# Kernel optimization log

Measured on AMD Instinct MI355X. Metric: run time of the kernel, lower is better.

The kernel has to match this reference:

```python
import jax, jax.numpy as jnp
import numpy as np
from jax import lax

B, C, H, W = 32, 64, 112, 112
ALPHA, BETA1, BETA2 = 0.25, 1.0, 1.0

# STE sign for weights (DifferntiableSign): fwd = +/-1, bwd mask |w|<=1 (w in [-1,1))
@jax.custom_vjp
def dsign(w):
    return jnp.where(w >= 0, 1.0, -1.0).astype(w.dtype)
def _dsign_fwd(w):
    return dsign(w), w
def _dsign_bwd(w, g):
    return (g * ((w < 1) & (w >= -1)).astype(g.dtype),)
dsign.defvjp(_dsign_fwd, _dsign_bwd)

# ReActNet BinaryActivation: fwd = sign(x), bwd piecewise-polynomial STE
@jax.custom_vjp
def bin_act(x):
    return jnp.where(x >= 0, 1.0, -1.0).astype(x.dtype)
def _ba_fwd(x):
    return bin_act(x), x
def _ba_bwd(x, g):
    slope = jnp.where((x >= -1) & (x < 0), 2.0 + 2.0 * x,
             jnp.where((x >= 0) & (x < 1), 2.0 - 2.0 * x, 0.0))
    return (g * slope.astype(g.dtype),)
bin_act.defvjp(_ba_fwd, _ba_bwd)

def scaled_sign_conv(x, w):
    # per-output-channel scale = mean(|w|) over (in, kh, kw)
    scale = jnp.mean(jnp.abs(w), axis=(1, 2, 3), keepdims=True)
    wb = scale * dsign(w)
    return lax.conv_general_dilated(x, wb, window_strides=(1, 1),
                                    padding=((1, 1), (1, 1)),
                                    dimension_numbers=("NCHW", "OIHW", "NCHW"))

def add_bias(x, b):
    return x + b[None, :, None, None]

def prelu(x, a):
    return jnp.where(x >= 0, x, a[None, :, None, None] * x)

def setup_inputs() -> dict:
    key = jax.random.key(0)
    ks = jax.random.split(key, 12)
    x = jax.random.normal(ks[0], (B, C, H, W), dtype=jnp.float32)
    # conv weights: symmetric uniform in [-1e-3, 1e-3] so signs are nontrivial
    w3 = (jax.random.uniform(ks[1], (C, C, 3, 3)) - 0.5) * 0.002
    w_pw = (jax.random.uniform(ks[2], (C, C, 3, 3)) - 0.5) * 0.002
    b11 = jax.random.normal(ks[3], (C,)) * 0.01
    b12 = jax.random.normal(ks[4], (C,)) * 0.01
    b13 = jax.random.normal(ks[5], (C,)) * 0.01
    b21 = jax.random.normal(ks[6], (C,)) * 0.01
    b22 = jax.random.normal(ks[7], (C,)) * 0.01
    b23 = jax.random.normal(ks[8], (C,)) * 0.01
    a1 = jax.random.uniform(ks[9], (C,), minval=0.1, maxval=0.4)
    a2 = jax.random.uniform(ks[10], (C,), minval=0.1, maxval=0.4)
    return {"x": x, "w3": w3, "w_pw": w_pw, "b11": b11, "b12": b12, "b13": b13,
            "b21": b21, "b22": b22, "b23": b23, "a1": a1, "a2": a2}

def reference(x, w3, w_pw, b11, b12, b13, b21, b22, b23, a1, a2):
    x_in = x * BETA1
    out1 = add_bias(x_in, b11)            # move11
    out1 = bin_act(out1)
    out1 = scaled_sign_conv(out1, w3)     # binary_3x3
    out1 = x + out1 * ALPHA               # stride==1: residual is original x
    out1 = add_bias(out1, b12)            # move12
    out1 = prelu(out1, a1)
    out1 = add_bias(out1, b13)            # move13
    out1_in = out1 * BETA2
    out2 = add_bias(out1_in, b21)         # move21
    out2 = bin_act(out2)
    out2 = scaled_sign_conv(out2, w_pw)   # binary_pw (3x3 per given defaults)
    out2 = out2 * ALPHA + out1
    out2 = add_bias(out2, b22)            # move22
    out2 = prelu(out2, a2)
    out2 = add_bias(out2, b23)            # move23
    return out2
```

## Files before the change

### kernel.cpp

```cpp
#include <hip/hip_runtime.h>
#include <hip/hip_fp16.h>
#include <stdint.h>

#define Bn 32
#define Cc 64
#define Hh 112
#define Ww 112
#define HWp (Hh*Ww)
#define NPIX (Bn*HWp)
#define PW 114
#define PHW (PW*PW)
#define ALPHA 0.25f

#define WB1_OFF   0
#define WB2_OFF   4608
#define ASC1_OFF  9216
#define ASC2_OFF  9472
#define CI1_OFF   9728
#define CI2_OFF   12032
#define BITS1_OFF 16384
#define BITS2_OFF (16384 + 3326976)
#define OUT1H_OFF (16384 + 2*3326976)
#define WS_NEED   (OUT1H_OFF + (size_t)NPIX*Cc*2)

__global__ __launch_bounds__(64) void prep_weights(
        const float* __restrict__ w3, const float* __restrict__ wpw,
        uint64_t* __restrict__ wb1, uint64_t* __restrict__ wb2,
        float* __restrict__ asc1, float* __restrict__ asc2,
        int* __restrict__ ci1, int* __restrict__ ci2) {
    int b = blockIdx.x;
    int lane = threadIdx.x;
    const float* w  = (b < 64) ? w3   : wpw;
    uint64_t* wbits = (b < 64) ? wb1  : wb2;
    float*    ascp  = (b < 64) ? asc1 : asc2;
    int*      cip   = (b < 64) ? ci1  : ci2;
    int o = b & 63;
    const float* wp = w + ((size_t)o * Cc + lane) * 9;
    float v[9]; float asum = 0.f;
    #pragma unroll
    for (int t = 0; t < 9; ++t) { v[t] = wp[t]; asum += fabsf(v[t]); }
    uint64_t bal[9];
    #pragma unroll
    for (int t = 0; t < 9; ++t) bal[t] = __ballot(v[t] < 0.f);
    if (lane < 9) {
        wbits[o * 9 + lane] = bal[lane];
        int ty = lane, tr = ty / 3, tc = ty % 3;
        int sum = 0;
        #pragma unroll
        for (int t = 0; t < 9; ++t) {
            int r = t / 3, c = t % 3;
            bool inv = (tr == 0 && r == 0) || (tr == 2 && r == 2) ||
                       (tc == 0 && c == 0) || (tc == 2 && c == 2);
            if (inv) sum += 64 - 2 * (int)__popcll(bal[t]);
        }
        cip[o * 9 + ty] = 576 - sum;
    }
    #pragma unroll
    for (int off = 32; off > 0; off >>= 1) asum += __shfl_down(asum, off, 64);
    if (lane == 0) ascp[o] = ALPHA * asum * (1.f / 576.f);
}

__global__ __launch_bounds__(256) void pack1(const float* __restrict__ x,
                                             const float* __restrict__ b11,
                                             uint64_t* __restrict__ bits1,
                                             uint64_t* __restrict__ bits2) {
    int pc = blockIdx.x * 256 + threadIdx.x;
    if (pc >= PHW) return;
    int n = blockIdx.y;
    int ph = pc / PW, pw = pc - ph * PW;
    size_t bi = (size_t)n * PHW + pc;
    if (ph == 0 || ph == PW - 1 || pw == 0 || pw == PW - 1) {
        bits1[bi] = 0; bits2[bi] = 0;
        return;
    }
    int hw = (ph - 1) * Ww + (pw - 1);
    const float* xp = x + (size_t)n * Cc * HWp + hw;
    uint64_t m = 0;
    #pragma unroll 1
    for (int cc = 0; cc < Cc; cc += 16) {
        float v[16];
        #pragma unroll
        for (int j = 0; j < 16; ++j) v[j] = xp[(size_t)(cc + j) * HWp];
        #pragma unroll
        for (int j = 0; j < 16; ++j)
            if (v[j] + b11[cc + j] < 0.f) m |= (1ull << (cc + j));
    }
    bits1[bi] = m;
}

template <typename OutT>
__global__ __launch_bounds__(256) void conv1_ep(
        const float* __restrict__ x, const uint64_t* __restrict__ bits1,
        const uint64_t* __restrict__ wb, const float* __restrict__ asc,
        const int* __restrict__ cint,
        const float* __restrict__ b12, const float* __restrict__ a1,
        const float* __restrict__ b13, const float* __restrict__ b21,
        OutT* __restrict__ out1, uint64_t* __restrict__ bits2) {
    __shared__ int lci[Cc * 12];
    for (int i = threadIdx.x; i < Cc * 9; i += 256) {
        int o = i / 9, ty = i - o * 9;
        lci[o * 12 + ty] = cint[i];
    }
    __syncthreads();

    int hw = blockIdx.x * 256 + threadIdx.x;
    int n = blockIdx.y;
    int h = hw / Ww, w = hw - h * Ww;
    int t9 = ((h == 0) ? 0 : (h == Hh - 1) ? 6 : 3) +
             ((w == 0) ? 0 : (w == Ww - 1) ? 2 : 1);

    const uint64_t* bp = bits1 + (size_t)n * PHW + (h + 1) * PW + (w + 1);
    uint64_t w00 = bp[-PW - 1], w01 = bp[-PW], w02 = bp[-PW + 1];
    uint64_t w10 = bp[-1],      w11 = bp[0],   w12 = bp[1];
    uint64_t w20 = bp[PW - 1],  w21 = bp[PW],  w22 = bp[PW + 1];

    const float* xp = x + (size_t)n * Cc * HWp + hw;
    OutT* op = out1 + (size_t)n * Cc * HWp + hw;
    uint64_t m2 = 0;

    float xv[8], xn[8];
    #pragma unroll
    for (int j = 0; j < 8; ++j) xv[j] = xp[(size_t)j * HWp];

    #pragma unroll 1
    for (int oc = 0; oc < Cc; oc += 8) {
        #pragma unroll
        for (int j = 0; j < 8; ++j) xn[j] = xp[(size_t)((oc + 8 + j) & 63) * HWp];
        #pragma unroll
        for (int j = 0; j < 8; ++j) {
            int o = oc + j;
            const uint64_t* wo = wb + o * 9;
            int s;
            s  = (int)__popcll(w00 ^ wo[0]);
            s += (int)__popcll(w01 ^ wo[1]);
            s += (int)__popcll(w02 ^ wo[2]);
            s += (int)__popcll(w10 ^ wo[3]);
            s += (int)__popcll(w11 ^ wo[4]);
            s += (int)__popcll(w12 ^ wo[5]);
            s += (int)__popcll(w20 ^ wo[6]);
            s += (int)__popcll(w21 ^ wo[7]);
            s += (int)__popcll(w22 ^ wo[8]);
            int m = lci[o * 12 + t9] - (s << 1);
            float v = fmaf(asc[o], (float)m, xv[j]);
            v += b12[o];
            v = v >= 0.f ? v : a1[o] * v;
            v += b13[o];
            op[(size_t)o * HWp] = (OutT)v;
            if (v + b21[o] < 0.f) m2 |= (1ull << o);
        }
        #pragma unroll
        for (int j = 0; j < 8; ++j) xv[j] = xn[j];
    }
    bits2[(size_t)n * PHW + (h + 1) * PW + (w + 1)] = m2;
}

template <typename InT>
__global__ __launch_bounds__(256) void conv2_ep(
        const uint64_t* __restrict__ bits2, const InT* __restrict__ out1,
        const uint64_t* __restrict__ wb, const float* __restrict__ asc,
        const int* __restrict__ cint,
        const float* __restrict__ b22, const float* __restrict__ a2,
        const float* __restrict__ b23, float* __restrict__ out) {
    __shared__ int lci[Cc * 12];
    for (int i = threadIdx.x; i < Cc * 9; i += 256) {
        int o = i / 9, ty = i - o * 9;
        lci[o * 12 + ty] = cint[i];
    }
    __syncthreads();

    int hw = blockIdx.x * 256 + threadIdx.x;
    int n = blockIdx.y;
    int h = hw / Ww, w = hw - h * Ww;
    int t9 = ((h == 0) ? 0 : (h == Hh - 1) ? 6 : 3) +
             ((w == 0) ? 0 : (w == Ww - 1) ? 2 : 1);

    const uint64_t* bp = bits2 + (size_t)n * PHW + (h + 1) * PW + (w + 1);
    uint64_t w00 = bp[-PW - 1], w01 = bp[-PW], w02 = bp[-PW + 1];
    uint64_t w10 = bp[-1],      w11 = bp[0],   w12 = bp[1];
    uint64_t w20 = bp[PW - 1],  w21 = bp[PW],  w22 = bp[PW + 1];

    const InT* ip = out1 + (size_t)n * Cc * HWp + hw;
    float* op = out + (size_t)n * Cc * HWp + hw;

    InT rv[8], rn[8];
    #pragma unroll
    for (int j = 0; j < 8; ++j) rv[j] = ip[(size_t)j * HWp];

    #pragma unroll 1
    for (int oc = 0; oc < Cc; oc += 8) {
        #pragma unroll
        for (int j = 0; j < 8; ++j) rn[j] = ip[(size_t)((oc + 8 + j) & 63) * HWp];
        #pragma unroll
        for (int j = 0; j < 8; ++j) {
            int o = oc + j;
            const uint64_t* wo = wb + o * 9;
            int s;
            s  = (int)__popcll(w00 ^ wo[0]);
            s += (int)__popcll(w01 ^ wo[1]);
            s += (int)__popcll(w02 ^ wo[2]);
            s += (int)__popcll(w10 ^ wo[3]);
            s += (int)__popcll(w11 ^ wo[4]);
            s += (int)__popcll(w12 ^ wo[5]);
            s += (int)__popcll(w20 ^ wo[6]);
            s += (int)__popcll(w21 ^ wo[7]);
            s += (int)__popcll(w22 ^ wo[8]);
            int m = lci[o * 12 + t9] - (s << 1);
            float v = fmaf(asc[o], (float)m, (float)rv[j]);
            v += b22[o];
            v = v >= 0.f ? v : a2[o] * v;
            v += b23[o];
            op[(size_t)o * HWp] = v;
        }
        #pragma unroll
        for (int j = 0; j < 8; ++j) rv[j] = rn[j];
    }
}

extern "C" void kernel_launch(void* const* d_in, const int* in_sizes, int n_in,
                              void* d_out, int out_size, void* d_ws, size_t ws_size,
                              hipStream_t stream) {
    const float* x    = (const float*)d_in[0];
    const float* w3   = (const float*)d_in[1];
    const float* wpw  = (const float*)d_in[2];
    const float* b11  = (const float*)d_in[3];
    const float* b12  = (const float*)d_in[4];
    const float* b13  = (const float*)d_in[5];
    const float* b21  = (const float*)d_in[6];
    const float* b22  = (const float*)d_in[7];
    const float* b23  = (const float*)d_in[8];
    const float* a1   = (const float*)d_in[9];
    const float* a2   = (const float*)d_in[10];

    char* ws = (char*)d_ws;
    uint64_t* wb1   = (uint64_t*)(ws + WB1_OFF);
    uint64_t* wb2   = (uint64_t*)(ws + WB2_OFF);
    float*    asc1  = (float*)(ws + ASC1_OFF);
    float*    asc2  = (float*)(ws + ASC2_OFF);
    int*      ci1   = (int*)(ws + CI1_OFF);
    int*      ci2   = (int*)(ws + CI2_OFF);
    uint64_t* bits1 = (uint64_t*)(ws + BITS1_OFF);
    uint64_t* bits2 = (uint64_t*)(ws + BITS2_OFF);
    float*    out   = (float*)d_out;

    dim3 pgrid((PHW + 255) / 256, Bn);
    dim3 cgrid(HWp / 256, Bn);

    prep_weights<<<128, 64, 0, stream>>>(w3, wpw, wb1, wb2, asc1, asc2, ci1, ci2);
    pack1<<<pgrid, 256, 0, stream>>>(x, b11, bits1, bits2);

    if (ws_size >= WS_NEED) {
        __half* out1h = (__half*)(ws + OUT1H_OFF);
        conv1_ep<__half><<<cgrid, 256, 0, stream>>>(x, bits1, wb1, asc1, ci1,
                                                    b12, a1, b13, b21, out1h, bits2);
        conv2_ep<__half><<<cgrid, 256, 0, stream>>>(bits2, out1h, wb2, asc2, ci2,
                                                    b22, a2, b23, out);
    } else {
        conv1_ep<float><<<cgrid, 256, 0, stream>>>(x, bits1, wb1, asc1, ci1,
                                                   b12, a1, b13, b21, out, bits2);
        conv2_ep<float><<<cgrid, 256, 0, stream>>>(bits2, out, wb2, asc2, ci2,
                                                   b22, a2, b23, out);
    }
}
```

Measured before the change: 294.1 us.

## Split channels across grid z and separate interior from border pixels

Adds a grid z dimension so each block handles 32 of the 64 channels, with bit masks written as 32-bit halves of the 64-bit words. This doubles the number of blocks available for parallelism. Interior pixels now use a constant 576 correction and skip the shared-memory correction table, while the 444 border pixels get their own blocks that read the table from global memory. The register prefetch of the next channel group is dropped, and each thread's neighbour bit loads are now done twice, once per channel half.

Result: slower. 337.1 us (+14.6%).

```diff
diff --git a/kernel.cpp b/kernel.cpp
--- a/kernel.cpp
+++ b/kernel.cpp
@@ -10,6 +10,10 @@
 #define NPIX (Bn*HWp)
 #define PW 114
 #define PHW (PW*PW)
+#define IW 110
+#define IPX (IW*IW)
+#define NINT_BLK 48
+#define BPX 444
 #define ALPHA 0.25f
 
 #define WB1_OFF   0
@@ -62,30 +66,37 @@
 
 __global__ __launch_bounds__(256) void pack1(const float* __restrict__ x,
                                              const float* __restrict__ b11,
-                                             uint64_t* __restrict__ bits1,
-                                             uint64_t* __restrict__ bits2) {
+                                             uint32_t* __restrict__ bits1_32,
+                                             uint32_t* __restrict__ bits2_32) {
     int pc = blockIdx.x * 256 + threadIdx.x;
     if (pc >= PHW) return;
-    int n = blockIdx.y;
+    int n = blockIdx.y, z = blockIdx.z, cbase = z * 32;
     int ph = pc / PW, pw = pc - ph * PW;
-    size_t bi = (size_t)n * PHW + pc;
+    size_t wi = ((size_t)n * PHW + pc) * 2 + z;
     if (ph == 0 || ph == PW - 1 || pw == 0 || pw == PW - 1) {
-        bits1[bi] = 0; bits2[bi] = 0;
+        bits1_32[wi] = 0; bits2_32[wi] = 0;
         return;
     }
     int hw = (ph - 1) * Ww + (pw - 1);
-    const float* xp = x + (size_t)n * Cc * HWp + hw;
-    uint64_t m = 0;
+    const float* xp = x + ((size_t)n * Cc + cbase) * HWp + hw;
+    uint32_t m = 0;
     #pragma unroll 1
-    for (int cc = 0; cc < Cc; cc += 16) {
+    for (int cc = 0; cc < 32; cc += 16) {
         float v[16];
         #pragma unroll
         for (int j = 0; j < 16; ++j) v[j] = xp[(size_t)(cc + j) * HWp];
         #pragma unroll
         for (int j = 0; j < 16; ++j)
-            if (v[j] + b11[cc + j] < 0.f) m |= (1ull << (cc + j));
-    }
-    bits1[bi] = m;
+            if (v[j] + b11[cbase + cc + j] < 0.f) m |= (1u << (cc + j));
+    }
+    bits1_32[wi] = m;
+}
+
+__device__ __forceinline__ void border_map(int p, int& h, int& w) {
+    if (p < 112)      { h = 0;   w = p; }
+    else if (p < 224) { h = 111; w = p - 112; }
+    else if (p < 334) { h = 1 + (p - 224); w = 0; }
+    else              { h = 1 + (p - 334); w = 111; }
 }
 
 template <typename OutT>
@@ -95,63 +106,67 @@
         const int* __restrict__ cint,
         const float* __restrict__ b12, const float* __restrict__ a1,
         const float* __restrict__ b13, const float* __restrict__ b21,
-        OutT* __restrict__ out1, uint64_t* __restrict__ bits2) {
-    __shared__ int lci[Cc * 12];
-    for (int i = threadIdx.x; i < Cc * 9; i += 256) {
-        int o = i / 9, ty = i - o * 9;
-        lci[o * 12 + ty] = cint[i];
-    }
-    __syncthreads();
-
-    int hw = blockIdx.x * 256 + threadIdx.x;
-    int n = blockIdx.y;
-    int h = hw / Ww, w = hw - h * Ww;
-    int t9 = ((h == 0) ? 0 : (h == Hh - 1) ? 6 : 3) +
+        OutT* __restrict__ out1, uint32_t* __restrict__ bits2_32) {
+    int n = blockIdx.y, z = blockIdx.z, obase = z * 32;
+    int bx = blockIdx.x;
+    bool interior = (bx < NINT_BLK);
+    int h, w, t9 = 4;
+    if (interior) {
+        int p = bx * 256 + threadIdx.x;
+        if (p >= IPX) return;
+        int ph = p / IW;
+        h = 1 + ph; w = 1 + (p - ph * IW);
+    } else {
+        int p = (bx - NINT_BLK) * 256 + threadIdx.x;
+        if (p >= BPX) return;
+        border_map(p, h, w);
+        t9 = ((h == 0) ? 0 : (h == Hh - 1) ? 6 : 3) +
              ((w == 0) ? 0 : (w == Ww - 1) ? 2 : 1);
-
+    }
+    int hw = h * Ww + w;
     const uint64_t* bp = bits1 + (size_t)n * PHW + (h + 1) * PW + (w + 1);
     uint64_t w00 = bp[-PW - 1], w01 = bp[-PW], w02 = bp[-PW + 1];
     uint64_t w10 = bp[-1],      w11 = bp[0],   w12 = bp[1];
     uint64_t w20 = bp[PW - 1],  w21 = bp[PW],  w22 = bp[PW + 1];
 
-    const float* xp = x + (size_t)n * Cc * HWp + hw;
-    OutT* op = out1 + (size_t)n * Cc * HWp + hw;
-    uint64_t m2 = 0;
-
-    float xv[8], xn[8];
-    #pragma unroll
-    for (int j = 0; j < 8; ++j) xv[j] = xp[(size_t)j * HWp];
-
-    #pragma unroll 1
-    for (int oc = 0; oc < Cc; oc += 8) {
-        #pragma unroll
-        for (int j = 0; j < 8; ++j) xn[j] = xp[(size_t)((oc + 8 + j) & 63) * HWp];
-        #pragma unroll
-        for (int j = 0; j < 8; ++j) {
-            int o = oc + j;
-            const uint64_t* wo = wb + o * 9;
-            int s;
-            s  = (int)__popcll(w00 ^ wo[0]);
-            s += (int)__popcll(w01 ^ wo[1]);
-            s += (int)__popcll(w02 ^ wo[2]);
-            s += (int)__popcll(w10 ^ wo[3]);
-            s += (int)__popcll(w11 ^ wo[4]);
-            s += (int)__popcll(w12 ^ wo[5]);
-            s += (int)__popcll(w20 ^ wo[6]);
-            s += (int)__popcll(w21 ^ wo[7]);
-            s += (int)__popcll(w22 ^ wo[8]);
-            int m = lci[o * 12 + t9] - (s << 1);
-            float v = fmaf(asc[o], (float)m, xv[j]);
-            v += b12[o];
-            v = v >= 0.f ? v : a1[o] * v;
-            v += b13[o];
-            op[(size_t)o * HWp] = (OutT)v;
-            if (v + b21[o] < 0.f) m2 |= (1ull << o);
+    const float* xp = x + ((size_t)n * Cc + obase) * HWp + hw;
+    OutT* op = out1 + ((size_t)n * Cc + obase) * HWp + hw;
+    uint32_t m2 = 0;
+
+    auto body = [&](auto base_of) {
+        #pragma unroll 1
+        for (int jc = 0; jc < 32; jc += 8) {
+            float xv[8];
+            #pragma unroll
+            for (int j = 0; j < 8; ++j) xv[j] = xp[(size_t)(jc + j) * HWp];
+            #pragma unroll
+            for (int j = 0; j < 8; ++j) {
+                int o = obase + jc + j;
+                const uint64_t* wo = wb + o * 9;
+                int s;
+                s  = (int)__popcll(w00 ^ wo[0]);
+                s += (int)__popcll(w01 ^ wo[1]);
+                s += (int)__popcll(w02 ^ wo[2]);
+                s += (int)__popcll(w10 ^ wo[3]);
+                s += (int)__popcll(w11 ^ wo[4]);
+                s += (int)__popcll(w12 ^ wo[5]);
+                s += (int)__popcll(w20 ^ wo[6]);
+                s += (int)__popcll(w21 ^ wo[7]);
+                s += (int)__popcll(w22 ^ wo[8]);
+                int m = base_of(o) - (s << 1);
+                float v = fmaf(asc[o], (float)m, xv[j]);
+                v += b12[o];
+                v = v >= 0.f ? v : a1[o] * v;
+                v += b13[o];
+                op[(size_t)(jc + j) * HWp] = (OutT)v;
+                if (v + b21[o] < 0.f) m2 |= (1u << (jc + j));
+            }
         }
-        #pragma unroll
-        for (int j = 0; j < 8; ++j) xv[j] = xn[j];
-    }
-    bits2[(size_t)n * PHW + (h + 1) * PW + (w + 1)] = m2;
+    };
+    if (interior) body([&](int) { return 576; });
+    else          body([&](int o) { return cint[o * 9 + t9]; });
+
+    bits2_32[((size_t)n * PHW + (h + 1) * PW + (w + 1)) * 2 + z] = m2;
 }
 
 template <typename InT>
@@ -161,59 +176,62 @@
         const int* __restrict__ cint,
         const float* __restrict__ b22, const float* __restrict__ a2,
         const float* __restrict__ b23, float* __restrict__ out) {
-    __shared__ int lci[Cc * 12];
-    for (int i = threadIdx.x; i < Cc * 9; i += 256) {
-        int o = i / 9, ty = i - o * 9;
-        lci[o * 12 + ty] = cint[i];
-    }
-    __syncthreads();
-
-    int hw = blockIdx.x * 256 + threadIdx.x;
-    int n = blockIdx.y;
-    int h = hw / Ww, w = hw - h * Ww;
-    int t9 = ((h == 0) ? 0 : (h == Hh - 1) ? 6 : 3) +
+    int n = blockIdx.y, z = blockIdx.z, obase = z * 32;
+    int bx = blockIdx.x;
+    bool interior = (bx < NINT_BLK);
+    int h, w, t9 = 4;
+    if (interior) {
+        int p = bx * 256 + threadIdx.x;
+        if (p >= IPX) return;
+        int ph = p / IW;
+        h = 1 + ph; w = 1 + (p - ph * IW);
+    } else {
+        int p = (bx - NINT_BLK) * 256 + threadIdx.x;
+        if (p >= BPX) return;
+        border_map(p, h, w);
+        t9 = ((h == 0) ? 0 : (h == Hh - 1) ? 6 : 3) +
              ((w == 0) ? 0 : (w == Ww - 1) ? 2 : 1);
-
+    }
+    int hw = h * Ww + w;
     const uint64_t* bp = bits2 + (size_t)n * PHW + (h + 1) * PW + (w + 1);
     uint64_t w00 = bp[-PW - 1], w01 = bp[-PW], w02 = bp[-PW + 1];
     uint64_t w10 = bp[-1],      w11 = bp[0],   w12 = bp[1];
     uint64_t w20 = bp[PW - 1],  w21 = bp[PW],  w22 = bp[PW + 1];
 
-    const InT* ip = out1 + (size_t)n * Cc * HWp + hw;
-    float* op = out + (size_t)n * Cc * HWp + hw;
-
-    InT rv[8], rn[8];
-    #pragma unroll
-    for (int j = 0; j < 8; ++j) rv[j] = ip[(size_t)j * HWp];
-
-    #pragma unroll 1
-    for (int oc = 0; oc < Cc; oc += 8) {
-        #pragma unroll
-        for (int j = 0; j < 8; ++j) rn[j] = ip[(size_t)((oc + 8 + j) & 63) * HWp];
-        #pragma unroll
-        for (int j = 0; j < 8; ++j) {
-            int o = oc + j;
-            const uint64_t* wo = wb + o * 9;
-            int s;
-            s  = (int)__popcll(w00 ^ wo[0]);
-            s += (int)__popcll(w01 ^ wo[1]);
-            s += (int)__popcll(w02 ^ wo[2]);
-            s += (int)__popcll(w10 ^ wo[3]);
-            s += (int)__popcll(w11 ^ wo[4]);
-            s += (int)__popcll(w12 ^ wo[5]);
-            s += (int)__popcll(w20 ^ wo[6]);
-            s += (int)__popcll(w21 ^ wo[7]);
-            s += (int)__popcll(w22 ^ wo[8]);
-            int m = lci[o * 12 + t9] - (s << 1);
-            float v = fmaf(asc[o], (float)m, (float)rv[j]);
-            v += b22[o];
-            v = v >= 0.f ? v : a2[o] * v;
-            v += b23[o];
-            op[(size_t)o * HWp] = v;
+    const InT* ip = out1 + ((size_t)n * Cc + obase) * HWp + hw;
+    float* op = out + ((size_t)n * Cc + obase) * HWp + hw;
+
+    auto body = [&](auto base_of) {
+        #pragma unroll 1
+        for (int jc = 0; jc < 32; jc += 8) {
+            InT rv[8];
+            #pragma unroll
+            for (int j = 0; j < 8; ++j) rv[j] = ip[(size_t)(jc + j) * HWp];
+            #pragma unroll
+            for (int j = 0; j < 8; ++j) {
+                int o = obase + jc + j;
+                const uint64_t* wo = wb + o * 9;
+                int s;
+                s  = (int)__popcll(w00 ^ wo[0]);
+                s += (int)__popcll(w01 ^ wo[1]);
+                s += (int)__popcll(w02 ^ wo[2]);
+                s += (int)__popcll(w10 ^ wo[3]);
+                s += (int)__popcll(w11 ^ wo[4]);
+                s += (int)__popcll(w12 ^ wo[5]);
+                s += (int)__popcll(w20 ^ wo[6]);
+                s += (int)__popcll(w21 ^ wo[7]);
+                s += (int)__popcll(w22 ^ wo[8]);
+                int m = base_of(o) - (s << 1);
+                float v = fmaf(asc[o], (float)m, (float)rv[j]);
+                v += b22[o];
+                v = v >= 0.f ? v : a2[o] * v;
+                v += b23[o];
+                op[(size_t)(jc + j) * HWp] = v;
+            }
         }
-        #pragma unroll
-        for (int j = 0; j < 8; ++j) rv[j] = rn[j];
-    }
+    };
+    if (interior) body([&](int) { return 576; });
+    else          body([&](int o) { return cint[o * 9 + t9]; });
 }
 
 extern "C" void kernel_launch(void* const* d_in, const int* in_sizes, int n_in,
@@ -242,21 +260,23 @@
     uint64_t* bits2 = (uint64_t*)(ws + BITS2_OFF);
     float*    out   = (float*)d_out;
 
-    dim3 pgrid((PHW + 255) / 256, Bn);
-    dim3 cgrid(HWp / 256, Bn);
+    dim3 pgrid((PHW + 255) / 256, Bn, 2);
+    dim3 cgrid(NINT_BLK + 2, Bn, 2);
 
     prep_weights<<<128, 64, 0, stream>>>(w3, wpw, wb1, wb2, asc1, asc2, ci1, ci2);
-    pack1<<<pgrid, 256, 0, stream>>>(x, b11, bits1, bits2);
+    pack1<<<pgrid, 256, 0, stream>>>(x, b11, (uint32_t*)bits1, (uint32_t*)bits2);
 
     if (ws_size >= WS_NEED) {
         __half* out1h = (__half*)(ws + OUT1H_OFF);
         conv1_ep<__half><<<cgrid, 256, 0, stream>>>(x, bits1, wb1, asc1, ci1,
-                                                    b12, a1, b13, b21, out1h, bits2);
+                                                    b12, a1, b13, b21, out1h,
+                                                    (uint32_t*)bits2);
         conv2_ep<__half><<<cgrid, 256, 0, stream>>>(bits2, out1h, wb2, asc2, ci2,
                                                     b22, a2, b23, out);
     } else {
         conv1_ep<float><<<cgrid, 256, 0, stream>>>(x, bits1, wb1, asc1, ci1,
-                                                   b12, a1, b13, b21, out, bits2);
+                                                   b12, a1, b13, b21, out,
+                                                   (uint32_t*)bits2);
         conv2_ep<float><<<cgrid, 256, 0, stream>>>(bits2, out, wb2, asc2, ci2,
                                                    b22, a2, b23, out);
     }
```
